# Kernel tuning notes

Measured on AMD Instinct MI355X. Metric: run time of the kernel, lower is better.

## Reference

```python
import jax, jax.numpy as jnp
from jax import lax
import numpy as np

WS = 5  # window_size
H = 6   # hidden_size
IN = 3 * WS  # 15
OUT = 2


def setup_inputs() -> dict:
    key = jax.random.key(0)
    k1, k2, k3, k4, k5 = jax.random.split(key, 5)
    B, T = 8192, 1024
    one_full_traj = jax.random.normal(k1, (B, T, 3), dtype=jnp.float32)
    # nn.Linear-style params: y = x @ W.T + b
    W1 = jax.random.normal(k2, (H, IN), dtype=jnp.float32) * (1.0 / np.sqrt(IN))
    b1 = jax.random.normal(k3, (H,), dtype=jnp.float32) * 0.05
    W2 = jax.random.normal(k4, (OUT, H), dtype=jnp.float32) * (1.0 / np.sqrt(H))
    b2 = jax.random.normal(k5, (OUT,), dtype=jnp.float32) * 0.05
    return {"one_full_traj": one_full_traj, "W1": W1, "b1": b1, "W2": W2, "b2": b2}


def reference(one_full_traj, W1, b1, W2, b2):
    ws = WS
    B, T, _ = one_full_traj.shape

    def mlp(x):  # [B, 3*ws] -> [B, 2]
        return jnp.tanh(x @ W1.T + b1) @ W2.T + b2

    def make_inp(seq):  # [B, ws, 3] -> [B, 3*ws], channel-major per original cat order
        return jnp.transpose(seq, (0, 2, 1)).reshape(B, 3 * ws)

    # step 0
    out = mlp(make_inp(one_full_traj[:, :ws, :]))[:, None, :]  # [B, 1, 2]

    # warm-up loop t = 1 .. ws-1 (small fixed Python loop, matches original indexing)
    for t in range(1, ws):
        n = out.shape[1]  # == t
        tmp = jnp.concatenate(
            [one_full_traj[:, ws + (t - 1):ws + (t - 1) + n, 0:1], out], axis=2
        )  # [B, t, 3]
        seq = jnp.concatenate([one_full_traj[:, t:ws, :], tmp], axis=1)  # [B, ws, 3]
        out = jnp.concatenate([out, mlp(make_inp(seq))[:, None, :]], axis=1)

    # sliding window of the last ws predictions as carry.
    u = one_full_traj[:, :, 0]  # control channel, [B, T]

    def step(win, t):
        uw = lax.dynamic_slice_in_dim(u, t, ws, axis=1)  # [B, ws]
        seq = jnp.concatenate([uw[:, :, None], win], axis=2)  # [B, ws, 3]
        pred = mlp(make_inp(seq))  # [B, 2]
        win = jnp.concatenate([win[:, 1:, :], pred[:, None, :]], axis=1)
        return win, pred

    ts = jnp.arange(ws, T - ws)
    _, preds = lax.scan(step, out, ts)  # preds: [T-2*ws, B, 2]
    return jnp.concatenate([out, jnp.transpose(preds, (1, 0, 2))], axis=1)  # [B, T-ws, 2]
```

## Files before the change

### kernel.cpp

```cpp
#include <hip/hip_runtime.h>
#include <math.h>

#define TLEN  1024
#define NSTEP 1019
#define CHUNK 128
#define STAGE (CHUNK + 8)

template <int CTRL>
__device__ __forceinline__ float dpp_add(float v) {
    union { int i; float f; } in, out;
    in.f = v;
    out.i = __builtin_amdgcn_update_dpp(0, in.i, CTRL, 0xF, 0xF, false);
    return v + out.f;
}
__device__ __forceinline__ float sum8(float v) {
    v = dpp_add<0xB1>(v);
    v = dpp_add<0x4E>(v);
    v = dpp_add<0x141>(v);
    return v;
}

__global__ __launch_bounds__(64) void MLP_or_nextstep_kernel(
    const float* __restrict__ traj,
    const float* __restrict__ W1,
    const float* __restrict__ b1,
    const float* __restrict__ W2,
    const float* __restrict__ b2,
    float* __restrict__ out)
{
    __shared__ float lds_u[STAGE][8];

    const int lane = threadIdx.x;
    const int g    = lane >> 3;
    const int n    = lane & 7;
    const int bstart = blockIdx.x * 8;
    const int b = bstart + g;

    const float* __restrict__ base = traj + (size_t)b * (TLEN * 3);
    float2* outb = (float2*)out + (size_t)b * NSTEP;
    const bool is_store_lane = (n == 0);

    const int nr = (n < 6) ? n : 5;
    float w1row[15], b1r;
#pragma unroll
    for (int j = 0; j < 15; ++j) w1row[j] = 2.0f * W1[nr * 15 + j];
    b1r = 2.0f * b1[nr];
    const float w2a_l = (n < 6) ? W2[n]     : 0.0f;
    const float w2b_l = (n < 6) ? W2[6 + n] : 0.0f;
    const float b2a = b2[0], b2c = b2[1];

    auto mlp = [&](const float* __restrict__ x, float& ya, float& yb) {
        float z0 = w1row[0] * x[0];
        float z1 = w1row[5] * x[5];
        float z2 = fmaf(w1row[10], x[10], b1r);
#pragma unroll
        for (int j = 1; j < 5; ++j) {
            z0 = fmaf(w1row[j],      x[j],      z0);
            z1 = fmaf(w1row[5 + j],  x[5 + j],  z1);
            z2 = fmaf(w1row[10 + j], x[10 + j], z2);
        }
        float z = (z0 + z1) + z2;
        float e = __expf(z);
        float h = fmaf(-2.0f, __builtin_amdgcn_rcpf(e + 1.0f), 1.0f);
        float sa = sum8(h * w2a_l);
        float sb = sum8(h * w2b_l);
        ya = sa + b2a;
        yb = sb + b2c;
    };

    float uu[12], vv[5], wc[5];
#pragma unroll
    for (int i = 0; i < 12; ++i) uu[i] = base[i * 3];
#pragma unroll
    for (int i = 0; i < 5; ++i) { vv[i] = base[i * 3 + 1]; wc[i] = base[i * 3 + 2]; }

    float pa[5], pb[5];
    {
        float x[15] = {uu[0],uu[1],uu[2],uu[3],uu[4],
                       vv[0],vv[1],vv[2],vv[3],vv[4],
                       wc[0],wc[1],wc[2],wc[3],wc[4]};
        mlp(x, pa[0], pb[0]);
    }
    {
        float x[15] = {uu[1],uu[2],uu[3],uu[4],uu[5],
                       vv[1],vv[2],vv[3],vv[4],pa[0],
                       wc[1],wc[2],wc[3],wc[4],pb[0]};
        mlp(x, pa[1], pb[1]);
    }
    {
        float x[15] = {uu[2],uu[3],uu[4],uu[6],uu[7],
                       vv[2],vv[3],vv[4],pa[0],pa[1],
                       wc[2],wc[3],wc[4],pb[0],pb[1]};
        mlp(x, pa[2], pb[2]);
    }
    {
        float x[15] = {uu[3],uu[4],uu[7],uu[8],uu[9],
                       vv[3],vv[4],pa[0],pa[1],pa[2],
                       wc[3],wc[4],pb[0],pb[1],pb[2]};
        mlp(x, pa[3], pb[3]);
    }
    {
        float x[15] = {uu[4],uu[8],uu[9],uu[10],uu[11],
                       vv[4],pa[0],pa[1],pa[2],pa[3],
                       wc[4],pb[0],pb[1],pb[2],pb[3]};
        mlp(x, pa[4], pb[4]);
    }
    if (is_store_lane) {
#pragma unroll
        for (int i = 0; i < 5; ++i) outb[i] = make_float2(pa[i], pb[i]);
    }

    float aw[5], bw[5];
#pragma unroll
    for (int i = 0; i < 5; ++i) { aw[i] = pa[i]; bw[i] = pb[i]; }

    const int s_elem = lane & 7;
    const int s_row  = lane >> 3;
    const float* __restrict__ sbase = traj + (size_t)(bstart + s_elem) * (TLEN * 3);

    for (int t0 = 5; t0 < NSTEP; t0 += CHUNK) {
        int len = NSTEP - t0; if (len > CHUNK) len = CHUNK;

        for (int r0 = 0; r0 < STAGE; r0 += 8) {
            int ti = t0 + r0 + s_row;
            if (ti > TLEN - 1) ti = TLEN - 1;
            const float* gp = sbase + (size_t)ti * 3;
            __builtin_amdgcn_global_load_lds(
                (const __attribute__((address_space(1))) void*)gp,
                (__attribute__((address_space(3))) void*)&lds_u[r0][0],
                4, 0, 0);
        }
        __syncthreads();

        float uwin[8];
#pragma unroll
        for (int i = 0; i < 8; ++i) uwin[i] = lds_u[i][g];

#pragma unroll 2
        for (int c = 0; c < len; ++c) {
            float unext = lds_u[c + 8][g];

            float x[15] = {uwin[0],uwin[1],uwin[2],uwin[3],uwin[4],
                           aw[0],aw[1],aw[2],aw[3],aw[4],
                           bw[0],bw[1],bw[2],bw[3],bw[4]};
            float ya, yb;
            mlp(x, ya, yb);
            if (is_store_lane) outb[t0 + c] = make_float2(ya, yb);

#pragma unroll
            for (int i = 0; i < 7; ++i) uwin[i] = uwin[i + 1];
#pragma unroll
            for (int i = 0; i < 4; ++i) { aw[i] = aw[i + 1]; bw[i] = bw[i + 1]; }
            aw[4] = ya; bw[4] = yb;
            uwin[7] = unext;
        }
        __syncthreads();
    }
}

extern "C" void kernel_launch(void* const* d_in, const int* in_sizes, int n_in,
                              void* d_out, int out_size, void* d_ws, size_t ws_size,
                              hipStream_t stream) {
    const float* traj = (const float*)d_in[0];
    const float* W1   = (const float*)d_in[1];
    const float* b1   = (const float*)d_in[2];
    const float* W2   = (const float*)d_in[3];
    const float* b2   = (const float*)d_in[4];
    float* out = (float*)d_out;

    const int grid = 8192 / 8;
    MLP_or_nextstep_kernel<<<grid, 64, 0, stream>>>(traj, W1, b1, W2, b2, out);
}
```

Measured before the change: 284.0 us.

## Preload full control sequence into LDS and unroll recurrence with rotating windows

Stages the entire control channel (1024 steps × 8 batches) into LDS once at kernel start, replacing per-chunk staging and its barriers. The main loop is unrolled by five with modular register indexing, so the sliding window shifts become plain register renaming. tanh now uses exp2 with the log2e factor folded into W1, and b2 plus the affine part of tanh are folded into per-lane constants ahead of the DPP reduction. LDS use grows to 32KB per 64-thread block, which may limit occupancy.

Measured after the change: 265.3 us. -6.6%, faster.

```diff
diff --git a/kernel.cpp b/kernel.cpp
--- a/kernel.cpp
+++ b/kernel.cpp
@@ -3,8 +3,6 @@
 
 #define TLEN  1024
 #define NSTEP 1019
-#define CHUNK 128
-#define STAGE (CHUNK + 8)
 
 template <int CTRL>
 __device__ __forceinline__ float dpp_add(float v) {
@@ -18,6 +16,14 @@
     v = dpp_add<0x4E>(v);
     v = dpp_add<0x141>(v);
     return v;
+}
+
+__device__ __forceinline__ float fast_exp2(float z) {
+#if __has_builtin(__builtin_amdgcn_exp2f)
+    return __builtin_amdgcn_exp2f(z);
+#else
+    return exp2f(z);
+#endif
 }
 
 __global__ __launch_bounds__(64) void MLP_or_nextstep_kernel(
@@ -28,7 +34,7 @@
     const float* __restrict__ b2,
     float* __restrict__ out)
 {
-    __shared__ float lds_u[STAGE][8];
+    __shared__ float lds_u[TLEN][8];
 
     const int lane = threadIdx.x;
     const int g    = lane >> 3;
@@ -40,14 +46,31 @@
     float2* outb = (float2*)out + (size_t)b * NSTEP;
     const bool is_store_lane = (n == 0);
 
+    {
+        const int s_elem = lane & 7;
+        const int s_row  = lane >> 3;
+        const float* __restrict__ sbase = traj + (size_t)(bstart + s_elem) * (TLEN * 3);
+        for (int j = 0; j < TLEN / 8; ++j) {
+            const float* gp = sbase + (size_t)(8 * j + s_row) * 3;
+            __builtin_amdgcn_global_load_lds(
+                (const __attribute__((address_space(1))) void*)gp,
+                (__attribute__((address_space(3))) void*)&lds_u[8 * j][0],
+                4, 0, 0);
+        }
+    }
+
+    const float KK = 2.8853900817779268f;
     const int nr = (n < 6) ? n : 5;
     float w1row[15], b1r;
 #pragma unroll
-    for (int j = 0; j < 15; ++j) w1row[j] = 2.0f * W1[nr * 15 + j];
-    b1r = 2.0f * b1[nr];
+    for (int j = 0; j < 15; ++j) w1row[j] = KK * W1[nr * 15 + j];
+    b1r = KK * b1[nr];
     const float w2a_l = (n < 6) ? W2[n]     : 0.0f;
     const float w2b_l = (n < 6) ? W2[6 + n] : 0.0f;
-    const float b2a = b2[0], b2c = b2[1];
+    const float bias_a = (n == 6) ? b2[0] : 0.0f;
+    const float bias_b = (n == 7) ? b2[1] : 0.0f;
+    const float c1a = -2.0f * w2a_l, c0a = w2a_l + bias_a;
+    const float c1b = -2.0f * w2b_l, c0b = w2b_l + bias_b;
 
     auto mlp = [&](const float* __restrict__ x, float& ya, float& yb) {
         float z0 = w1row[0] * x[0];
@@ -60,12 +83,9 @@
             z2 = fmaf(w1row[10 + j], x[10 + j], z2);
         }
         float z = (z0 + z1) + z2;
-        float e = __expf(z);
-        float h = fmaf(-2.0f, __builtin_amdgcn_rcpf(e + 1.0f), 1.0f);
-        float sa = sum8(h * w2a_l);
-        float sb = sum8(h * w2b_l);
-        ya = sa + b2a;
-        yb = sb + b2c;
+        float r = __builtin_amdgcn_rcpf(fast_exp2(z) + 1.0f);
+        ya = sum8(fmaf(c1a, r, c0a));
+        yb = sum8(fmaf(c1b, r, c0b));
     };
 
     float uu[12], vv[5], wc[5];
@@ -110,52 +130,62 @@
         for (int i = 0; i < 5; ++i) outb[i] = make_float2(pa[i], pb[i]);
     }
 
+    __syncthreads();
+
     float aw[5], bw[5];
 #pragma unroll
     for (int i = 0; i < 5; ++i) { aw[i] = pa[i]; bw[i] = pb[i]; }
 
-    const int s_elem = lane & 7;
-    const int s_row  = lane >> 3;
-    const float* __restrict__ sbase = traj + (size_t)(bstart + s_elem) * (TLEN * 3);
-
-    for (int t0 = 5; t0 < NSTEP; t0 += CHUNK) {
-        int len = NSTEP - t0; if (len > CHUNK) len = CHUNK;
-
-        for (int r0 = 0; r0 < STAGE; r0 += 8) {
-            int ti = t0 + r0 + s_row;
-            if (ti > TLEN - 1) ti = TLEN - 1;
-            const float* gp = sbase + (size_t)ti * 3;
-            __builtin_amdgcn_global_load_lds(
-                (const __attribute__((address_space(1))) void*)gp,
-                (__attribute__((address_space(3))) void*)&lds_u[r0][0],
-                4, 0, 0);
-        }
-        __syncthreads();
-
-        float uwin[8];
-#pragma unroll
-        for (int i = 0; i < 8; ++i) uwin[i] = lds_u[i][g];
-
-#pragma unroll 2
-        for (int c = 0; c < len; ++c) {
-            float unext = lds_u[c + 8][g];
-
-            float x[15] = {uwin[0],uwin[1],uwin[2],uwin[3],uwin[4],
-                           aw[0],aw[1],aw[2],aw[3],aw[4],
-                           bw[0],bw[1],bw[2],bw[3],bw[4]};
-            float ya, yb;
-            mlp(x, ya, yb);
-            if (is_store_lane) outb[t0 + c] = make_float2(ya, yb);
-
-#pragma unroll
-            for (int i = 0; i < 7; ++i) uwin[i] = uwin[i + 1];
-#pragma unroll
-            for (int i = 0; i < 4; ++i) { aw[i] = aw[i + 1]; bw[i] = bw[i + 1]; }
-            aw[4] = ya; bw[4] = yb;
-            uwin[7] = unext;
-        }
-        __syncthreads();
-    }
+    const float* up = &lds_u[5][g];
+    float2* op = outb + 5;
+
+#define STEP_BODY(s, UN)                                                     \
+    {                                                                        \
+        float z0 = w1row[0] * UN[s];                                         \
+        float z1 = w1row[5] * aw[(s) % 5];                                   \
+        float z2 = fmaf(w1row[10], bw[(s) % 5], b1r);                        \
+        z0 = fmaf(w1row[1], UN[s + 1], z0);                                  \
+        z1 = fmaf(w1row[6], aw[(s + 1) % 5], z1);                            \
+        z2 = fmaf(w1row[11], bw[(s + 1) % 5], z2);                           \
+        z0 = fmaf(w1row[2], UN[s + 2], z0);                                  \
+        z1 = fmaf(w1row[7], aw[(s + 2) % 5], z1);                            \
+        z2 = fmaf(w1row[12], bw[(s + 2) % 5], z2);                           \
+        z0 = fmaf(w1row[3], UN[s + 3], z0);                                  \
+        z1 = fmaf(w1row[8], aw[(s + 3) % 5], z1);                            \
+        z2 = fmaf(w1row[13], bw[(s + 3) % 5], z2);                           \
+        z0 = fmaf(w1row[4], UN[s + 4], z0);                                  \
+        z1 = fmaf(w1row[9], aw[(s + 4) % 5], z1);                            \
+        z2 = fmaf(w1row[14], bw[(s + 4) % 5], z2);                           \
+        float z = (z0 + z1) + z2;                                            \
+        float r = __builtin_amdgcn_rcpf(fast_exp2(z) + 1.0f);                \
+        float ya = sum8(fmaf(c1a, r, c0a));                                  \
+        float yb = sum8(fmaf(c1b, r, c0b));                                  \
+        if (is_store_lane) op[s] = make_float2(ya, yb);                      \
+        aw[(s) % 5] = ya; bw[(s) % 5] = yb;                                  \
+    }
+
+    for (int grp = 0; grp < 202; ++grp) {
+        float un[9];
+#pragma unroll
+        for (int i = 0; i < 9; ++i) un[i] = up[8 * i];
+        STEP_BODY(0, un)
+        STEP_BODY(1, un)
+        STEP_BODY(2, un)
+        STEP_BODY(3, un)
+        STEP_BODY(4, un)
+        up += 40;
+        op += 5;
+    }
+    {
+        float un[8];
+#pragma unroll
+        for (int i = 0; i < 8; ++i) un[i] = up[8 * i];
+        STEP_BODY(0, un)
+        STEP_BODY(1, un)
+        STEP_BODY(2, un)
+        STEP_BODY(3, un)
+    }
+#undef STEP_BODY
 }
 
 extern "C" void kernel_launch(void* const* d_in, const int* in_sizes, int n_in,
```
